# Performance work log

Measured on AMD Instinct MI355X. Metric: run time of the kernel, lower is better.

## Reference

```python
import jax, jax.numpy as jnp
import numpy as np

H = 64      # hidden_dim
NH = 4      # attention heads
HD = H // NH
NC = 13     # num_classes
NF = 8      # node features


def setup_inputs() -> dict:
    key = jax.random.key(0)
    ks = iter(jax.random.split(key, 32))
    B, T, N, E = 4, 16, 4096, 32768
    s = 0.05
    d = {}
    d["node_features"] = jax.random.normal(next(ks), (B, T, N, NF), jnp.float32)
    d["edge_index"] = jax.random.randint(next(ks), (T, 2, E), 0, N, jnp.int32)
    # spatial conv (Linear(NF,H), ReLU, Linear(H,H))
    d["sc_w1"] = jax.random.normal(next(ks), (H, NF), jnp.float32) * s
    d["sc_b1"] = jnp.zeros((H,), jnp.float32)
    d["sc_w2"] = jax.random.normal(next(ks), (H, H), jnp.float32) * s
    d["sc_b2"] = jnp.zeros((H,), jnp.float32)
    # 2-layer LSTM (pytorch gate order i,f,g,o)
    for l in range(2):
        d[f"lstm_w_ih{l}"] = jax.random.normal(next(ks), (4 * H, H), jnp.float32) * s
        d[f"lstm_w_hh{l}"] = jax.random.normal(next(ks), (4 * H, H), jnp.float32) * s
        d[f"lstm_b_ih{l}"] = jnp.zeros((4 * H,), jnp.float32)
        d[f"lstm_b_hh{l}"] = jnp.zeros((4 * H,), jnp.float32)
    # MultiheadAttention in_proj / out_proj
    d["attn_w_in"] = jax.random.normal(next(ks), (3 * H, H), jnp.float32) * s
    d["attn_b_in"] = jnp.zeros((3 * H,), jnp.float32)
    d["attn_w_out"] = jax.random.normal(next(ks), (H, H), jnp.float32) * s
    d["attn_b_out"] = jnp.zeros((H,), jnp.float32)
    # predictor MLP (dropout inactive at eval)
    d["p_w1"] = jax.random.normal(next(ks), (2 * H, H), jnp.float32) * s
    d["p_b1"] = jnp.zeros((2 * H,), jnp.float32)
    d["p_w2"] = jax.random.normal(next(ks), (H, 2 * H), jnp.float32) * s
    d["p_b2"] = jnp.zeros((H,), jnp.float32)
    d["p_w3"] = jax.random.normal(next(ks), (NC, H), jnp.float32) * s
    d["p_b3"] = jnp.zeros((NC,), jnp.float32)
    return d


def _lstm_layer(x, w_ih, w_hh, b_ih, b_hh):
    # x: (T, BN, H_in) -> (T, BN, H)
    BN = x.shape[1]
    Hh = w_hh.shape[1]

    def step(carry, xt):
        h, c = carry
        z = xt @ w_ih.T + h @ w_hh.T + (b_ih + b_hh)
        i, f, g, o = jnp.split(z, 4, axis=-1)
        c = jax.nn.sigmoid(f) * c + jax.nn.sigmoid(i) * jnp.tanh(g)
        h = jax.nn.sigmoid(o) * jnp.tanh(c)
        return (h, c), h

    h0 = jnp.zeros((BN, Hh), x.dtype)
    _, ys = jax.lax.scan(step, (h0, h0), x)
    return ys


def _forward(node_features, edge_index, sc_w1, sc_b1, sc_w2, sc_b2,
             lstm_w_ih0, lstm_w_hh0, lstm_b_ih0, lstm_b_hh0,
             lstm_w_ih1, lstm_w_hh1, lstm_b_ih1, lstm_b_hh1,
             attn_w_in, attn_b_in, attn_w_out, attn_b_out,
             p_w1, p_b1, p_w2, p_b2, p_w3, p_b3):
    B, T, N, _ = node_features.shape
    # spatial conv applied to every (b,t,n)
    h = jax.nn.relu(jnp.einsum('btnf,hf->btnh', node_features, sc_w1) + sc_b1)
    h = jnp.einsum('btnh,gh->btng', h, sc_w2) + sc_b2  # (B,T,N,H)

    def agg_step(_, inp):
        h_t, edges = inp  # (B,N,H), (2,E)
        src, dst = edges[0], edges[1]
        msgs = h_t[:, src]  # (B,E,H) gathered from pre-update h_t (matches torch)
        ssum = jax.vmap(lambda m: jax.ops.segment_sum(m, dst, num_segments=N))(msgs)
        cnt = jax.ops.segment_sum(jnp.ones(dst.shape, h_t.dtype), dst, num_segments=N)
        mean = ssum / jnp.maximum(cnt, 1.0)[None, :, None]
        h_new = jnp.where(cnt[None, :, None] > 0, (h_t + mean) * 0.5, h_t)
        return None, h_new

    _, h_agg = jax.lax.scan(agg_step, None, (h.transpose(1, 0, 2, 3), edge_index))
    h = h_agg.transpose(1, 0, 2, 3)  # (B,T,N,H)

    # per-node temporal sequence: (T, B*N, H)
    x = h.transpose(0, 2, 1, 3).reshape(B * N, T, H).transpose(1, 0, 2)
    x = _lstm_layer(x, lstm_w_ih0, lstm_w_hh0, lstm_b_ih0, lstm_b_hh0)
    x = _lstm_layer(x, lstm_w_ih1, lstm_w_hh1, lstm_b_ih1, lstm_b_hh1)
    x = x.transpose(1, 0, 2)  # (BN,T,H)

    # multi-head self-attention (batch_first)
    qkv = x @ attn_w_in.T + attn_b_in
    q, k, v = jnp.split(qkv, 3, axis=-1)
    BN = q.shape[0]
    q = q.reshape(BN, T, NH, HD)
    k = k.reshape(BN, T, NH, HD)
    v = v.reshape(BN, T, NH, HD)
    scores = jnp.einsum('bthd,bshd->bhts', q, k) / jnp.sqrt(jnp.float32(HD)).astype(x.dtype)
    attn = jax.nn.softmax(scores, axis=-1)
    o = jnp.einsum('bhts,bshd->bthd', attn, v).reshape(BN, T, H)
    o = o @ attn_w_out.T + attn_b_out

    final = o[:, -1, :]  # (BN,H)
    z = jax.nn.relu(final @ p_w1.T + p_b1)
    z = jax.nn.relu(z @ p_w2.T + p_b2)
    logits = z @ p_w3.T + p_b3
    return logits.reshape(B, N, NC)


def reference(node_features, edge_index, sc_w1, sc_b1, sc_w2, sc_b2,
              lstm_w_ih0, lstm_w_hh0, lstm_b_ih0, lstm_b_hh0,
              lstm_w_ih1, lstm_w_hh1, lstm_b_ih1, lstm_b_hh1,
              attn_w_in, attn_b_in, attn_w_out, attn_b_out,
              p_w1, p_b1, p_w2, p_b2, p_w3, p_b3):
    return _forward(node_features, edge_index, sc_w1, sc_b1, sc_w2, sc_b2,
                    lstm_w_ih0, lstm_w_hh0, lstm_b_ih0, lstm_b_hh0,
                    lstm_w_ih1, lstm_w_hh1, lstm_b_ih1, lstm_b_hh1,
                    attn_w_in, attn_b_in, attn_w_out, attn_b_out,
                    p_w1, p_b1, p_w2, p_b2, p_w3, p_b3)
```

## Files before the change

kernel.cpp:

```cpp
#include <hip/hip_runtime.h>

constexpr int kB  = 4;
constexpr int kT  = 16;
constexpr int kN  = 4096;
constexpr int kBN = kB * kN;
constexpr int kE  = 32768;
constexpr int kNC = 13;

typedef _Float16 f16x8 __attribute__((ext_vector_type(8)));
typedef _Float16 f16x4 __attribute__((ext_vector_type(4)));
typedef float f32x4 __attribute__((ext_vector_type(4)));

__device__ __forceinline__ float sigm(float x) { return 1.f / (1.f + __expf(-x)); }
__device__ __forceinline__ float tanh_(float x) {
  float e = __expf(2.f * x);
  return 1.f - 2.f / (e + 1.f);
}

__device__ __forceinline__ f32x4 mm3(f16x8 ah, f16x8 al, f16x8 bh, f16x8 bl, f32x4 acc) {
  acc = __builtin_amdgcn_mfma_f32_16x16x32_f16(ah, bh, acc, 0, 0, 0);
  acc = __builtin_amdgcn_mfma_f32_16x16x32_f16(ah, bl, acc, 0, 0, 0);
  acc = __builtin_amdgcn_mfma_f32_16x16x32_f16(al, bh, acc, 0, 0, 0);
  return acc;
}

__device__ __forceinline__ void split8(const float* p, f16x8& hi, f16x8& lo) {
  float4 u0 = *(const float4*)p, u1 = *(const float4*)(p + 4);
  float vv[8] = {u0.x, u0.y, u0.z, u0.w, u1.x, u1.y, u1.z, u1.w};
#pragma unroll
  for (int j = 0; j < 8; ++j) {
    _Float16 hj = (_Float16)vv[j];
    hi[j] = hj;
    lo[j] = (_Float16)(vv[j] - (float)hj);
  }
}

__device__ __forceinline__ void split8T(const float* base, int kbase, int seq,
                                        f16x8& hi, f16x8& lo) {
  float vv[8];
#pragma unroll
  for (int j = 0; j < 8; ++j) vv[j] = base[(kbase + j) * 68 + seq];
#pragma unroll
  for (int j = 0; j < 8; ++j) {
    _Float16 hj = (_Float16)vv[j];
    hi[j] = hj;
    lo[j] = (_Float16)(vv[j] - (float)hj);
  }
}

__device__ __forceinline__ unsigned int packf(float v) {
  _Float16 h = (_Float16)v;
  _Float16 l = (_Float16)(v - (float)h);
  unsigned short uh = __builtin_bit_cast(unsigned short, h);
  unsigned short ul = __builtin_bit_cast(unsigned short, l);
  return (unsigned int)uh | ((unsigned int)ul << 16);
}
__device__ __forceinline__ float up2(unsigned int w) {
  _Float16 h = __builtin_bit_cast(_Float16, (unsigned short)(w & 0xFFFFu));
  _Float16 l = __builtin_bit_cast(_Float16, (unsigned short)(w >> 16));
  return (float)h + (float)l;
}
__device__ __forceinline__ void unpack8(const unsigned int* w, f16x8& hi, f16x8& lo) {
#pragma unroll
  for (int j = 0; j < 8; ++j) {
    hi[j] = __builtin_bit_cast(_Float16, (unsigned short)(w[j] & 0xFFFFu));
    lo[j] = __builtin_bit_cast(_Float16, (unsigned short)(w[j] >> 16));
  }
}

__global__ __launch_bounds__(256, 2) void conv_kernel(
    const float* __restrict__ nf, const float* __restrict__ w1,
    const float* __restrict__ b1, const float* __restrict__ w2,
    const float* __restrict__ b2, unsigned int* __restrict__ hpk) {
  __shared__ unsigned int act[256 * 68];
  int tid = threadIdx.x;
  int w = tid >> 6, lane = tid & 63;
  int q = lane >> 4, i = lane & 15;
  int flat0 = blockIdx.x * 256;
  int bb = flat0 >> 16;
  int t = (flat0 >> 12) & 15;
  int n0 = flat0 & 4095;

  f16x8 w1h[4], w1l[4];
  f16x8 w2h[4][2], w2l[4][2];
  float bias1[4], bias2[4];
#pragma unroll
  for (int nt = 0; nt < 4; ++nt) {
    int n = nt * 16 + i;
    if (q == 0) split8(w1 + n * 8, w1h[nt], w1l[nt]);
    else { w1h[nt] = (f16x8)0; w1l[nt] = (f16x8)0; }
#pragma unroll
    for (int ks = 0; ks < 2; ++ks)
      split8(w2 + n * 64 + ks * 32 + q * 8, w2h[nt][ks], w2l[nt][ks]);
    bias1[nt] = b1[n];
    bias2[nt] = b2[n];
  }

  f16x8 xh[4], xl[4];
#pragma unroll
  for (int Mt = 0; Mt < 4; ++Mt) {
    if (q == 0)
      split8(nf + (size_t)(flat0 + w * 64 + Mt * 16 + i) * 8, xh[Mt], xl[Mt]);
    else { xh[Mt] = (f16x8)0; xl[Mt] = (f16x8)0; }
  }
#pragma unroll
  for (int Mt = 0; Mt < 4; ++Mt)
#pragma unroll
    for (int nt = 0; nt < 4; ++nt) {
      f32x4 acc = {bias1[nt], bias1[nt], bias1[nt], bias1[nt]};
      acc = mm3(xh[Mt], xl[Mt], w1h[nt], w1l[nt], acc);
#pragma unroll
      for (int r = 0; r < 4; ++r)
        act[(w * 64 + Mt * 16 + q * 4 + r) * 68 + nt * 16 + i] =
            packf(fmaxf(acc[r], 0.f));
    }
  __syncthreads();

  f32x4 acc2[4][4];
#pragma unroll
  for (int Mt = 0; Mt < 4; ++Mt)
#pragma unroll
    for (int nt = 0; nt < 4; ++nt) {
      acc2[Mt][nt][0] = bias2[nt]; acc2[Mt][nt][1] = bias2[nt];
      acc2[Mt][nt][2] = bias2[nt]; acc2[Mt][nt][3] = bias2[nt];
    }
#pragma unroll
  for (int ks = 0; ks < 2; ++ks)
#pragma unroll
    for (int Mt = 0; Mt < 4; ++Mt) {
      const unsigned int* p = &act[(w * 64 + Mt * 16 + i) * 68 + ks * 32 + q * 8];
      unsigned int wd[8];
#pragma unroll
      for (int j = 0; j < 4; ++j) {
        uint2 u = *(const uint2*)(p + j * 2);
        wd[2 * j] = u.x; wd[2 * j + 1] = u.y;
      }
      f16x8 ah, al;
      unpack8(wd, ah, al);
#pragma unroll
      for (int nt = 0; nt < 4; ++nt)
        acc2[Mt][nt] = mm3(ah, al, w2h[nt][ks], w2l[nt][ks], acc2[Mt][nt]);
    }
  __syncthreads();
#pragma unroll
  for (int Mt = 0; Mt < 4; ++Mt)
#pragma unroll
    for (int nt = 0; nt < 4; ++nt)
#pragma unroll
      for (int r = 0; r < 4; ++r)
        act[(w * 64 + Mt * 16 + q * 4 + r) * 68 + nt * 16 + i] =
            packf(acc2[Mt][nt][r]);
  __syncthreads();
  size_t tbase = ((size_t)t * kBN + (size_t)bb * kN + n0) * 64;
#pragma unroll
  for (int k = 0; k < 16; ++k) {
    int d0 = (k * 256 + tid) * 4;
    int node = d0 >> 6, ch = d0 & 63;
    uint2 a = *(const uint2*)&act[node * 68 + ch];
    uint2 b = *(const uint2*)&act[node * 68 + ch + 2];
    uint4 vv = {a.x, a.y, b.x, b.y};
    *(uint4*)(hpk + tbase + d0) = vv;
  }
}

__global__ __launch_bounds__(256) void count_kernel(
    const int* __restrict__ ei, int* __restrict__ cnt) {
  int i = blockIdx.x * 256 + threadIdx.x;
  int t = i >> 15, e = i & (kE - 1);
  int dst = ei[t * 2 * kE + kE + e];
  atomicAdd(&cnt[t * kN + dst], 1);
}

__global__ __launch_bounds__(1024) void scan_kernel(
    const int* __restrict__ cnt, int* __restrict__ off, int* __restrict__ cur) {
  __shared__ int sdata[1024];
  int t = blockIdx.x;
  int tid = threadIdx.x;
  const int* c = cnt + t * kN;
  int v0 = c[tid * 4], v1 = c[tid * 4 + 1], v2 = c[tid * 4 + 2], v3 = c[tid * 4 + 3];
  int s = v0 + v1 + v2 + v3;
  sdata[tid] = s;
  __syncthreads();
  for (int d = 1; d < 1024; d <<= 1) {
    int add = (tid >= d) ? sdata[tid - d] : 0;
    __syncthreads();
    sdata[tid] += add;
    __syncthreads();
  }
  int base = sdata[tid] - s;
  int o = t * kN + tid * 4;
  off[o] = base;            cur[o] = base;
  off[o + 1] = base + v0;   cur[o + 1] = base + v0;
  off[o + 2] = base + v0 + v1;        cur[o + 2] = base + v0 + v1;
  off[o + 3] = base + v0 + v1 + v2;   cur[o + 3] = base + v0 + v1 + v2;
}

__global__ __launch_bounds__(256) void place_kernel(
    const int* __restrict__ ei, int* __restrict__ cur, int* __restrict__ csr) {
  int i = blockIdx.x * 256 + threadIdx.x;
  int t = i >> 15, e = i & (kE - 1);
  int src = ei[t * 2 * kE + e];
  int dst = ei[t * 2 * kE + kE + e];
  int pos = atomicAdd(&cur[t * kN + dst], 1);
  csr[t * kE + pos] = src;
}

__global__ __launch_bounds__(256) void gather_kernel(
    const unsigned int* __restrict__ hpk, const int* __restrict__ csr,
    const int* __restrict__ off, const int* __restrict__ cnt,
    _Float16* __restrict__ xhi, _Float16* __restrict__ xlo) {
  int wv = blockIdx.x * 4 + (threadIdx.x >> 6);
  int t = wv >> 12, d = wv & (kN - 1);
  int lane = threadIdx.x & 63;
  int b = lane >> 4, cq = lane & 15;
  int o = off[t * kN + d];
  int c = cnt[t * kN + d];
  size_t tb = ((size_t)t * kBN + (size_t)b * kN) * 64 + cq * 4;
  const int* cs = csr + t * kE + o;
  float s[4] = {0.f, 0.f, 0.f, 0.f};
  int j = 0;
  for (; j + 4 <= c; j += 4) {
    int i0 = cs[j], i1 = cs[j + 1], i2 = cs[j + 2], i3 = cs[j + 3];
    uint4 v0 = *(const uint4*)(hpk + tb + (size_t)i0 * 64);
    uint4 v1 = *(const uint4*)(hpk + tb + (size_t)i1 * 64);
    uint4 v2 = *(const uint4*)(hpk + tb + (size_t)i2 * 64);
    uint4 v3 = *(const uint4*)(hpk + tb + (size_t)i3 * 64);
    s[0] += up2(v0.x) + up2(v1.x) + up2(v2.x) + up2(v3.x);
    s[1] += up2(v0.y) + up2(v1.y) + up2(v2.y) + up2(v3.y);
    s[2] += up2(v0.z) + up2(v1.z) + up2(v2.z) + up2(v3.z);
    s[3] += up2(v0.w) + up2(v1.w) + up2(v2.w) + up2(v3.w);
  }
  for (; j < c; ++j) {
    int i0 = cs[j];
    uint4 v0 = *(const uint4*)(hpk + tb + (size_t)i0 * 64);
    s[0] += up2(v0.x); s[1] += up2(v0.y); s[2] += up2(v0.z); s[3] += up2(v0.w);
  }
  uint4 hv = *(const uint4*)(hpk + tb + (size_t)d * 64);
  float hvf[4] = {up2(hv.x), up2(hv.y), up2(hv.z), up2(hv.w)};
  f16x4 ohi, olo;
  float inv = (c > 0) ? 1.f / (float)c : 0.f;
#pragma unroll
  for (int u = 0; u < 4; ++u) {
    float ov = (c > 0) ? (hvf[u] + s[u] * inv) * 0.5f : hvf[u];
    _Float16 hi = (_Float16)ov;
    ohi[u] = hi;
    olo[u] = (_Float16)(ov - (float)hi);
  }
  *(f16x4*)(xhi + tb + (size_t)d * 64) = ohi;
  *(f16x4*)(xlo + tb + (size_t)d * 64) = olo;
}

__global__ __launch_bounds__(256, 2) void lstm_kernel(
    const _Float16* __restrict__ xhi, const _Float16* __restrict__ xlo,
    _Float16* __restrict__ yhi, _Float16* __restrict__ ylo,
    const float* __restrict__ wih, const float* __restrict__ whh,
    const float* __restrict__ bih, const float* __restrict__ bhh) {
  __shared__ _Float16 hfrag[2][2][2][2][512];
  int tid = threadIdx.x;
  int cb = tid >> 6, lane = tid & 63;
  int q = lane >> 4, i = lane & 15;
  int s0 = blockIdx.x * 32;

  f16x8 wr[2][4][2][2];
#pragma unroll
  for (int mat = 0; mat < 2; ++mat) {
    const float* W = mat ? whh : wih;
#pragma unroll
    for (int g = 0; g < 4; ++g) {
      int row = (g * 4 + cb) * 16 + i;
#pragma unroll
      for (int ks = 0; ks < 2; ++ks)
        split8(W + row * 64 + ks * 32 + q * 8, wr[mat][g][ks][0], wr[mat][g][ks][1]);
    }
  }
  int ch = cb * 16 + i;
  float bias4[4];
#pragma unroll
  for (int g = 0; g < 4; ++g) bias4[g] = bih[g * 64 + ch] + bhh[g * 64 + ch];
  float cst[2][4];
#pragma unroll
  for (int ml = 0; ml < 2; ++ml)
#pragma unroll
    for (int r = 0; r < 4; ++r) cst[ml][r] = 0.f;
  int ks2 = ch >> 5, q2 = (ch >> 3) & 3, j2 = ch & 7;
  int p = 0;

  for (int t = 0; t < kT; ++t) {
    f32x4 acc[2][4];
#pragma unroll
    for (int ml = 0; ml < 2; ++ml)
#pragma unroll
      for (int g = 0; g < 4; ++g) {
        acc[ml][g][0] = bias4[g]; acc[ml][g][1] = bias4[g];
        acc[ml][g][2] = bias4[g]; acc[ml][g][3] = bias4[g];
      }
#pragma unroll
    for (int ks = 0; ks < 2; ++ks) {
      f16x8 xah[2], xal[2];
#pragma unroll
      for (int ml = 0; ml < 2; ++ml) {
        size_t base = ((size_t)t * kBN + s0 + ml * 16 + i) * 64 + ks * 32 + q * 8;
        xah[ml] = *(const f16x8*)(xhi + base);
        xal[ml] = *(const f16x8*)(xlo + base);
      }
#pragma unroll
      for (int g = 0; g < 4; ++g)
#pragma unroll
        for (int ml = 0; ml < 2; ++ml)
          acc[ml][g] = mm3(xah[ml], xal[ml], wr[0][g][ks][0], wr[0][g][ks][1], acc[ml][g]);
    }
    if (t > 0) {
#pragma unroll
      for (int ks = 0; ks < 2; ++ks) {
        f16x8 hah[2], hal[2];
#pragma unroll
        for (int ml = 0; ml < 2; ++ml) {
          hah[ml] = *(const f16x8*)&hfrag[p][ml][ks][0][lane * 8];
          hal[ml] = *(const f16x8*)&hfrag[p][ml][ks][1][lane * 8];
        }
#pragma unroll
        for (int g = 0; g < 4; ++g)
#pragma unroll
          for (int ml = 0; ml < 2; ++ml)
            acc[ml][g] = mm3(hah[ml], hal[ml], wr[1][g][ks][0], wr[1][g][ks][1], acc[ml][g]);
      }
    }
#pragma unroll
    for (int ml = 0; ml < 2; ++ml)
#pragma unroll
      for (int r = 0; r < 4; ++r) {
        float zi = acc[ml][0][r], zf = acc[ml][1][r];
        float zg = acc[ml][2][r], zo = acc[ml][3][r];
        float ig = sigm(zi), fg = sigm(zf), gg = tanh_(zg), og = sigm(zo);
        float c = fg * cst[ml][r] + ig * gg;
        cst[ml][r] = c;
        float hv = og * tanh_(c);
        int row = q * 4 + r;
        size_t ob = ((size_t)t * kBN + s0 + ml * 16 + row) * 64 + ch;
        _Float16 hh = (_Float16)hv;
        _Float16 hl = (_Float16)(hv - (float)hh);
        yhi[ob] = hh;
        ylo[ob] = hl;
        int lane2 = q2 * 16 + row;
        hfrag[p ^ 1][ml][ks2][0][lane2 * 8 + j2] = hh;
        hfrag[p ^ 1][ml][ks2][1][lane2 * 8 + j2] = hl;
      }
    __syncthreads();
    p ^= 1;
  }
}

__device__ __forceinline__ void stage_frags64(const float* W, _Float16* base,
                                              int O, int tid) {
  int total = O * 16;
  for (int idx = tid; idx < total; idx += 256) {
    int r = idx >> 4, k4 = idx & 15;
    float4 v = *(const float4*)&W[r * 64 + k4 * 4];
    int k = k4 * 4;
    int nt = r >> 4, ii = r & 15, ks = k >> 5, qq = (k >> 3) & 3, j0 = k & 7;
    _Float16* dh = base + ((nt * 2 + ks) * 2) * 512 + (qq * 16 + ii) * 8 + j0;
    _Float16* dl = dh + 512;
    float vv[4] = {v.x, v.y, v.z, v.w};
#pragma unroll
    for (int u = 0; u < 4; ++u) {
      _Float16 hh = (_Float16)vv[u];
      dh[u] = hh;
      dl[u] = (_Float16)(vv[u] - (float)hh);
    }
  }
}

__device__ __forceinline__ void stage_frags128(const float* W, _Float16* base,
                                               int O, int tid) {
  int total = O * 32;
  for (int idx = tid; idx < total; idx += 256) {
    int r = idx >> 5, k4 = idx & 31;
    float4 v = *(const float4*)&W[r * 128 + k4 * 4];
    int k = k4 * 4;
    int nt = r >> 4, ii = r & 15, ks = k >> 5, qq = (k >> 3) & 3, j0 = k & 7;
    _Float16* dh = base + ((nt * 4 + ks) * 2) * 512 + (qq * 16 + ii) * 8 + j0;
    _Float16* dl = dh + 512;
    float vv[4] = {v.x, v.y, v.z, v.w};
#pragma unroll
    for (int u = 0; u < 4; ++u) {
      _Float16 hh = (_Float16)vv[u];
      dh[u] = hh;
      dl[u] = (_Float16)(vv[u] - (float)hh);
    }
  }
}

__global__ __launch_bounds__(256, 1) void head_kernel(
    const _Float16* __restrict__ xhi, const _Float16* __restrict__ xlo,
    const float* __restrict__ win, const float* __restrict__ bin,
    const float* __restrict__ wout, const float* __restrict__ bout,
    const float* __restrict__ pw1, const float* __restrict__ pb1,
    const float* __restrict__ pw2, const float* __restrict__ pb2,
    const float* __restrict__ pw3, const float* __restrict__ pb3,
    float* __restrict__ out) {
  __shared__ __align__(16) float smem[30720];
  _Float16* wb = (_Float16*)smem;
  float* buf = smem + 21504;

  int tid = threadIdx.x;
  int w = tid >> 6, lane = tid & 63;
  int q = lane >> 4, i = lane & 15;
  int s0 = blockIdx.x * 64;

  stage_frags64(win, wb, 64, tid);
  stage_frags64(win + 64 * 64, wb + 8192, 128, tid);
  __syncthreads();

  {
    f16x8 ah[2], al[2];
#pragma unroll
    for (int ks = 0; ks < 2; ++ks) {
      size_t base = ((size_t)15 * kBN + s0 + w * 16 + i) * 64 + ks * 32 + q * 8;
      ah[ks] = *(const f16x8*)(xhi + base);
      al[ks] = *(const f16x8*)(xlo + base);
    }
#pragma unroll
    for (int nt = 0; nt < 4; ++nt) {
      float bias = bin[nt * 16 + i];
      f32x4 acc = {bias, bias, bias, bias};
#pragma unroll
      for (int ks = 0; ks < 2; ++ks) {
        const _Float16* bp = wb + ((nt * 2 + ks) * 2) * 512 + lane * 8;
        acc = mm3(ah[ks], al[ks], *(const f16x8*)bp, *(const f16x8*)(bp + 512), acc);
      }
      *(float4*)&buf[(nt * 16 + i) * 68 + w * 16 + q * 4] = *(float4*)&acc;
    }
  }
  __syncthreads();
  float qreg[16];
#pragma unroll
  for (int d = 0; d < 16; ++d) qreg[d] = buf[(w * 16 + d) * 68 + lane];
  __syncthreads();

  float m = -1e30f, l = 0.f;
  float o[16];
#pragma unroll
  for (int d = 0; d < 16; ++d) o[d] = 0.f;

  for (int t = 0; t < kT; ++t) {
    f16x8 xah[4][2], xal[4][2];
#pragma unroll
    for (int Mt = 0; Mt < 4; ++Mt)
#pragma unroll
      for (int ks = 0; ks < 2; ++ks) {
        size_t base = ((size_t)t * kBN + s0 + Mt * 16 + i) * 64 + ks * 32 + q * 8;
        xah[Mt][ks] = *(const f16x8*)(xhi + base);
        xal[Mt][ks] = *(const f16x8*)(xlo + base);
      }
#pragma unroll
    for (int u = 0; u < 2; ++u) {
      int nt = 2 * w + u;
      float bias = bin[64 + nt * 16 + i];
      f16x8 bh[2], bl[2];
#pragma unroll
      for (int ks = 0; ks < 2; ++ks) {
        const _Float16* bp = wb + 8192 + ((nt * 2 + ks) * 2) * 512 + lane * 8;
        bh[ks] = *(const f16x8*)bp;
        bl[ks] = *(const f16x8*)(bp + 512);
      }
#pragma unroll
      for (int Mt = 0; Mt < 4; ++Mt) {
        f32x4 acc = {bias, bias, bias, bias};
#pragma unroll
        for (int ks = 0; ks < 2; ++ks)
          acc = mm3(xah[Mt][ks], xal[Mt][ks], bh[ks], bl[ks], acc);
        *(float4*)&buf[(nt * 16 + i) * 68 + Mt * 16 + q * 4] = *(float4*)&acc;
      }
    }
    __syncthreads();
    float sc = 0.f;
#pragma unroll
    for (int d = 0; d < 16; ++d) sc += qreg[d] * buf[(w * 16 + d) * 68 + lane];
    sc *= 0.25f;
    float mn = fmaxf(m, sc);
    float alpha = __expf(m - mn);
    float pp = __expf(sc - mn);
    l = l * alpha + pp;
#pragma unroll
    for (int d = 0; d < 16; ++d)
      o[d] = o[d] * alpha + pp * buf[(64 + w * 16 + d) * 68 + lane];
    m = mn;
    __syncthreads();
  }

  float linv = 1.f / l;
#pragma unroll
  for (int d = 0; d < 16; ++d) buf[(w * 16 + d) * 68 + lane] = o[d] * linv;
  __syncthreads();

  stage_frags64(wout, wb, 64, tid);
  stage_frags64(pw1, wb + 8192, 128, tid);
  stage_frags128(pw2, wb + 24576, 64, tid);
  for (int idx = tid; idx < 256; idx += 256) {
    int r = idx >> 4, k4 = idx & 15;
    float4 v = {0.f, 0.f, 0.f, 0.f};
    if (r < kNC) v = *(const float4*)&pw3[r * 64 + k4 * 4];
    int k = k4 * 4;
    int ks = k >> 5, qq = (k >> 3) & 3, j0 = k & 7;
    _Float16* dh = wb + 40960 + (ks * 2) * 512 + (qq * 16 + r) * 8 + j0;
    _Float16* dl = dh + 512;
    float vv[4] = {v.x, v.y, v.z, v.w};
#pragma unroll
    for (int u = 0; u < 4; ++u) {
      _Float16 hh = (_Float16)vv[u];
      dh[u] = hh;
      dl[u] = (_Float16)(vv[u] - (float)hh);
    }
  }
  __syncthreads();

  int seq = w * 16 + i;

  {
    f16x8 ah[2], al[2];
    split8T(buf, q * 8, seq, ah[0], al[0]);
    split8T(buf, 32 + q * 8, seq, ah[1], al[1]);
#pragma unroll
    for (int nt = 0; nt < 4; ++nt) {
      float bias = bout[nt * 16 + i];
      f32x4 acc = {bias, bias, bias, bias};
#pragma unroll
      for (int ks = 0; ks < 2; ++ks) {
        const _Float16* bp = wb + ((nt * 2 + ks) * 2) * 512 + lane * 8;
        acc = mm3(ah[ks], al[ks], *(const f16x8*)bp, *(const f16x8*)(bp + 512), acc);
      }
      *(float4*)&buf[4352 + (nt * 16 + i) * 68 + w * 16 + q * 4] = *(float4*)&acc;
    }
  }
  __syncthreads();

  {
    f16x8 ah[2], al[2];
    split8T(buf + 4352, q * 8, seq, ah[0], al[0]);
    split8T(buf + 4352, 32 + q * 8, seq, ah[1], al[1]);
    __syncthreads();
#pragma unroll
    for (int nt = 0; nt < 8; ++nt) {
      float bias = pb1[nt * 16 + i];
      f32x4 acc = {bias, bias, bias, bias};
#pragma unroll
      for (int ks = 0; ks < 2; ++ks) {
        const _Float16* bp = wb + 8192 + ((nt * 2 + ks) * 2) * 512 + lane * 8;
        acc = mm3(ah[ks], al[ks], *(const f16x8*)bp, *(const f16x8*)(bp + 512), acc);
      }
      f32x4 r4;
#pragma unroll
      for (int r = 0; r < 4; ++r) r4[r] = fmaxf(acc[r], 0.f);
      *(float4*)&buf[(nt * 16 + i) * 68 + w * 16 + q * 4] = *(float4*)&r4;
    }
  }
  __syncthreads();

  {
    f16x8 ah[4], al[4];
#pragma unroll
    for (int ks = 0; ks < 4; ++ks)
      split8T(buf, ks * 32 + q * 8, seq, ah[ks], al[ks]);
    __syncthreads();
#pragma unroll
    for (int nt = 0; nt < 4; ++nt) {
      float bias = pb2[nt * 16 + i];
      f32x4 acc = {bias, bias, bias, bias};
#pragma unroll
      for (int ks = 0; ks < 4; ++ks) {
        const _Float16* bp = wb + 24576 + ((nt * 4 + ks) * 2) * 512 + lane * 8;
        acc = mm3(ah[ks], al[ks], *(const f16x8*)bp, *(const f16x8*)(bp + 512), acc);
      }
      f32x4 r4;
#pragma unroll
      for (int r = 0; r < 4; ++r) r4[r] = fmaxf(acc[r], 0.f);
      *(float4*)&buf[(nt * 16 + i) * 68 + w * 16 + q * 4] = *(float4*)&r4;
    }
  }
  __syncthreads();

  {
    f16x8 ah[2], al[2];
    split8T(buf, q * 8, seq, ah[0], al[0]);
    split8T(buf, 32 + q * 8, seq, ah[1], al[1]);
    f32x4 acc = {0.f, 0.f, 0.f, 0.f};
#pragma unroll
    for (int ks = 0; ks < 2; ++ks) {
      const _Float16* bp = wb + 40960 + (ks * 2) * 512 + lane * 8;
      acc = mm3(ah[ks], al[ks], *(const f16x8*)bp, *(const f16x8*)(bp + 512), acc);
    }
    if (i < kNC) {
      float bb = pb3[i];
#pragma unroll
      for (int r = 0; r < 4; ++r)
        out[(size_t)(s0 + w * 16 + q * 4 + r) * kNC + i] = acc[r] + bb;
    }
  }
}

extern "C" void kernel_launch(void* const* d_in, const int* in_sizes, int n_in,
                              void* d_out, int out_size, void* d_ws, size_t ws_size,
                              hipStream_t stream) {
  const float* nf    = (const float*)d_in[0];
  const int*   ei    = (const int*)d_in[1];
  const float* sc_w1 = (const float*)d_in[2];
  const float* sc_b1 = (const float*)d_in[3];
  const float* sc_w2 = (const float*)d_in[4];
  const float* sc_b2 = (const float*)d_in[5];
  const float* wih0  = (const float*)d_in[6];
  const float* whh0  = (const float*)d_in[7];
  const float* bih0  = (const float*)d_in[8];
  const float* bhh0  = (const float*)d_in[9];
  const float* wih1  = (const float*)d_in[10];
  const float* whh1  = (const float*)d_in[11];
  const float* bih1  = (const float*)d_in[12];
  const float* bhh1  = (const float*)d_in[13];
  const float* win   = (const float*)d_in[14];
  const float* bin   = (const float*)d_in[15];
  const float* wout  = (const float*)d_in[16];
  const float* bout  = (const float*)d_in[17];
  const float* pw1   = (const float*)d_in[18];
  const float* pb1   = (const float*)d_in[19];
  const float* pw2   = (const float*)d_in[20];
  const float* pb2   = (const float*)d_in[21];
  const float* pw3   = (const float*)d_in[22];
  const float* pb3   = (const float*)d_in[23];
  float* out = (float*)d_out;

  const size_t NB = (size_t)kT * kBN * 64;
  unsigned int* Hpk = (unsigned int*)d_ws;
  _Float16* Ahi = (_Float16*)(Hpk + NB);
  _Float16* Alo = Ahi + NB;
  _Float16* Bhi = Alo + NB;
  _Float16* Blo = Bhi + NB;
  int* cnt = (int*)(Blo + NB);
  int* off = cnt + kT * kN;
  int* cur = off + kT * kN;
  int* csr = cur + kT * kN;

  hipMemsetAsync(cnt, 0, (size_t)kT * kN * sizeof(int), stream);

  conv_kernel<<<1024, 256, 0, stream>>>(nf, sc_w1, sc_b1, sc_w2, sc_b2, Hpk);
  count_kernel<<<2048, 256, 0, stream>>>(ei, cnt);
  scan_kernel<<<16, 1024, 0, stream>>>(cnt, off, cur);
  place_kernel<<<2048, 256, 0, stream>>>(ei, cur, csr);
  gather_kernel<<<16384, 256, 0, stream>>>(Hpk, csr, off, cnt, Bhi, Blo);
  lstm_kernel<<<512, 256, 0, stream>>>(Bhi, Blo, Ahi, Alo, wih0, whh0, bih0, bhh0);
  lstm_kernel<<<512, 256, 0, stream>>>(Ahi, Alo, Bhi, Blo, wih1, whh1, bih1, bhh1);
  head_kernel<<<256, 256, 0, stream>>>(Bhi, Blo, win, bin, wout, bout,
                                       pw1, pb1, pw2, pb2, pw3, pb3, out);
}
```

Before: 464.5 us.

## Fuse both LSTM layers into one wavefront-pipelined kernel via shared memory

Replaces the two per-layer LSTM launches with a single kernel that runs layer 0 and layer 1 in separate 256-thread groups of a 512-thread block. Layer 1 consumes layer 0's hidden state from shared memory one timestep behind. This removes the global write and re-read of the intermediate layer-0 sequence and one kernel launch. The cost is larger blocks with more register pressure, one extra pipeline step, and a shared barrier that couples the two layers' step latency.

```diff
diff --git a/kernel.cpp b/kernel.cpp
--- a/kernel.cpp
+++ b/kernel.cpp
@@ -250,21 +250,30 @@
   *(f16x4*)(xlo + tb + (size_t)d * 64) = olo;
 }
 
-__global__ __launch_bounds__(256, 2) void lstm_kernel(
+__global__ __launch_bounds__(512, 2) void lstm2_kernel(
     const _Float16* __restrict__ xhi, const _Float16* __restrict__ xlo,
     _Float16* __restrict__ yhi, _Float16* __restrict__ ylo,
-    const float* __restrict__ wih, const float* __restrict__ whh,
-    const float* __restrict__ bih, const float* __restrict__ bhh) {
-  __shared__ _Float16 hfrag[2][2][2][2][512];
+    const float* __restrict__ wih0, const float* __restrict__ whh0,
+    const float* __restrict__ bih0, const float* __restrict__ bhh0,
+    const float* __restrict__ wih1, const float* __restrict__ whh1,
+    const float* __restrict__ bih1, const float* __restrict__ bhh1) {
+  __shared__ _Float16 h1f[2][2][2][2][512];
+  __shared__ _Float16 h2f[2][2][2][2][512];
   int tid = threadIdx.x;
-  int cb = tid >> 6, lane = tid & 63;
+  int grp = tid >> 8;
+  int cb = (tid >> 6) & 3, lane = tid & 63;
   int q = lane >> 4, i = lane & 15;
   int s0 = blockIdx.x * 32;
 
+  const float* Wih = grp ? wih1 : wih0;
+  const float* Whh = grp ? whh1 : whh0;
+  const float* Bih = grp ? bih1 : bih0;
+  const float* Bhh = grp ? bhh1 : bhh0;
+
   f16x8 wr[2][4][2][2];
 #pragma unroll
   for (int mat = 0; mat < 2; ++mat) {
-    const float* W = mat ? whh : wih;
+    const float* W = mat ? Whh : Wih;
 #pragma unroll
     for (int g = 0; g < 4; ++g) {
       int row = (g * 4 + cb) * 16 + i;
@@ -276,7 +285,7 @@
   int ch = cb * 16 + i;
   float bias4[4];
 #pragma unroll
-  for (int g = 0; g < 4; ++g) bias4[g] = bih[g * 64 + ch] + bhh[g * 64 + ch];
+  for (int g = 0; g < 4; ++g) bias4[g] = Bih[g * 64 + ch] + Bhh[g * 64 + ch];
   float cst[2][4];
 #pragma unroll
   for (int ml = 0; ml < 2; ++ml)
@@ -285,66 +294,130 @@
   int ks2 = ch >> 5, q2 = (ch >> 3) & 3, j2 = ch & 7;
   int p = 0;
 
-  for (int t = 0; t < kT; ++t) {
-    f32x4 acc[2][4];
-#pragma unroll
-    for (int ml = 0; ml < 2; ++ml)
-#pragma unroll
-      for (int g = 0; g < 4; ++g) {
-        acc[ml][g][0] = bias4[g]; acc[ml][g][1] = bias4[g];
-        acc[ml][g][2] = bias4[g]; acc[ml][g][3] = bias4[g];
-      }
-#pragma unroll
-    for (int ks = 0; ks < 2; ++ks) {
-      f16x8 xah[2], xal[2];
-#pragma unroll
-      for (int ml = 0; ml < 2; ++ml) {
-        size_t base = ((size_t)t * kBN + s0 + ml * 16 + i) * 64 + ks * 32 + q * 8;
-        xah[ml] = *(const f16x8*)(xhi + base);
-        xal[ml] = *(const f16x8*)(xlo + base);
-      }
-#pragma unroll
-      for (int g = 0; g < 4; ++g)
+  for (int it = 0; it < kT + 1; ++it) {
+    if (grp == 0) {
+      if (it < kT) {
+        int t = it;
+        f32x4 acc[2][4];
 #pragma unroll
         for (int ml = 0; ml < 2; ++ml)
-          acc[ml][g] = mm3(xah[ml], xal[ml], wr[0][g][ks][0], wr[0][g][ks][1], acc[ml][g]);
-    }
-    if (t > 0) {
-#pragma unroll
-      for (int ks = 0; ks < 2; ++ks) {
-        f16x8 hah[2], hal[2];
-#pragma unroll
-        for (int ml = 0; ml < 2; ++ml) {
-          hah[ml] = *(const f16x8*)&hfrag[p][ml][ks][0][lane * 8];
-          hal[ml] = *(const f16x8*)&hfrag[p][ml][ks][1][lane * 8];
+#pragma unroll
+          for (int g = 0; g < 4; ++g) {
+            acc[ml][g][0] = bias4[g]; acc[ml][g][1] = bias4[g];
+            acc[ml][g][2] = bias4[g]; acc[ml][g][3] = bias4[g];
+          }
+#pragma unroll
+        for (int ks = 0; ks < 2; ++ks) {
+          f16x8 xah[2], xal[2];
+#pragma unroll
+          for (int ml = 0; ml < 2; ++ml) {
+            size_t base = ((size_t)t * kBN + s0 + ml * 16 + i) * 64 + ks * 32 + q * 8;
+            xah[ml] = *(const f16x8*)(xhi + base);
+            xal[ml] = *(const f16x8*)(xlo + base);
+          }
+#pragma unroll
+          for (int g = 0; g < 4; ++g)
+#pragma unroll
+            for (int ml = 0; ml < 2; ++ml)
+              acc[ml][g] = mm3(xah[ml], xal[ml], wr[0][g][ks][0], wr[0][g][ks][1], acc[ml][g]);
         }
-#pragma unroll
-        for (int g = 0; g < 4; ++g)
-#pragma unroll
-          for (int ml = 0; ml < 2; ++ml)
-            acc[ml][g] = mm3(hah[ml], hal[ml], wr[1][g][ks][0], wr[1][g][ks][1], acc[ml][g]);
-      }
-    }
-#pragma unroll
-    for (int ml = 0; ml < 2; ++ml)
-#pragma unroll
-      for (int r = 0; r < 4; ++r) {
-        float zi = acc[ml][0][r], zf = acc[ml][1][r];
-        float zg = acc[ml][2][r], zo = acc[ml][3][r];
-        float ig = sigm(zi), fg = sigm(zf), gg = tanh_(zg), og = sigm(zo);
-        float c = fg * cst[ml][r] + ig * gg;
-        cst[ml][r] = c;
-        float hv = og * tanh_(c);
-        int row = q * 4 + r;
-        size_t ob = ((size_t)t * kBN + s0 + ml * 16 + row) * 64 + ch;
-        _Float16 hh = (_Float16)hv;
-        _Float16 hl = (_Float16)(hv - (float)hh);
-        yhi[ob] = hh;
-        ylo[ob] = hl;
-        int lane2 = q2 * 16 + row;
-        hfrag[p ^ 1][ml][ks2][0][lane2 * 8 + j2] = hh;
-        hfrag[p ^ 1][ml][ks2][1][lane2 * 8 + j2] = hl;
-      }
+        if (t > 0) {
+#pragma unroll
+          for (int ks = 0; ks < 2; ++ks) {
+            f16x8 hah[2], hal[2];
+#pragma unroll
+            for (int ml = 0; ml < 2; ++ml) {
+              hah[ml] = *(const f16x8*)&h1f[p][ml][ks][0][lane * 8];
+              hal[ml] = *(const f16x8*)&h1f[p][ml][ks][1][lane * 8];
+            }
+#pragma unroll
+            for (int g = 0; g < 4; ++g)
+#pragma unroll
+              for (int ml = 0; ml < 2; ++ml)
+                acc[ml][g] = mm3(hah[ml], hal[ml], wr[1][g][ks][0], wr[1][g][ks][1], acc[ml][g]);
+          }
+        }
+#pragma unroll
+        for (int ml = 0; ml < 2; ++ml)
+#pragma unroll
+          for (int r = 0; r < 4; ++r) {
+            float zi = acc[ml][0][r], zf = acc[ml][1][r];
+            float zg = acc[ml][2][r], zo = acc[ml][3][r];
+            float ig = sigm(zi), fg = sigm(zf), gg = tanh_(zg), og = sigm(zo);
+            float c = fg * cst[ml][r] + ig * gg;
+            cst[ml][r] = c;
+            float hv = og * tanh_(c);
+            int row = q * 4 + r;
+            _Float16 hh = (_Float16)hv;
+            _Float16 hl = (_Float16)(hv - (float)hh);
+            int lane2 = q2 * 16 + row;
+            h1f[p ^ 1][ml][ks2][0][lane2 * 8 + j2] = hh;
+            h1f[p ^ 1][ml][ks2][1][lane2 * 8 + j2] = hl;
+          }
+      }
+    } else {
+      if (it >= 1) {
+        int t = it - 1;
+        f32x4 acc[2][4];
+#pragma unroll
+        for (int ml = 0; ml < 2; ++ml)
+#pragma unroll
+          for (int g = 0; g < 4; ++g) {
+            acc[ml][g][0] = bias4[g]; acc[ml][g][1] = bias4[g];
+            acc[ml][g][2] = bias4[g]; acc[ml][g][3] = bias4[g];
+          }
+#pragma unroll
+        for (int ks = 0; ks < 2; ++ks) {
+          f16x8 xah[2], xal[2];
+#pragma unroll
+          for (int ml = 0; ml < 2; ++ml) {
+            xah[ml] = *(const f16x8*)&h1f[p][ml][ks][0][lane * 8];
+            xal[ml] = *(const f16x8*)&h1f[p][ml][ks][1][lane * 8];
+          }
+#pragma unroll
+          for (int g = 0; g < 4; ++g)
+#pragma unroll
+            for (int ml = 0; ml < 2; ++ml)
+              acc[ml][g] = mm3(xah[ml], xal[ml], wr[0][g][ks][0], wr[0][g][ks][1], acc[ml][g]);
+        }
+        if (t > 0) {
+#pragma unroll
+          for (int ks = 0; ks < 2; ++ks) {
+            f16x8 hah[2], hal[2];
+#pragma unroll
+            for (int ml = 0; ml < 2; ++ml) {
+              hah[ml] = *(const f16x8*)&h2f[p][ml][ks][0][lane * 8];
+              hal[ml] = *(const f16x8*)&h2f[p][ml][ks][1][lane * 8];
+            }
+#pragma unroll
+            for (int g = 0; g < 4; ++g)
+#pragma unroll
+              for (int ml = 0; ml < 2; ++ml)
+                acc[ml][g] = mm3(hah[ml], hal[ml], wr[1][g][ks][0], wr[1][g][ks][1], acc[ml][g]);
+          }
+        }
+#pragma unroll
+        for (int ml = 0; ml < 2; ++ml)
+#pragma unroll
+          for (int r = 0; r < 4; ++r) {
+            float zi = acc[ml][0][r], zf = acc[ml][1][r];
+            float zg = acc[ml][2][r], zo = acc[ml][3][r];
+            float ig = sigm(zi), fg = sigm(zf), gg = tanh_(zg), og = sigm(zo);
+            float c = fg * cst[ml][r] + ig * gg;
+            cst[ml][r] = c;
+            float hv = og * tanh_(c);
+            int row = q * 4 + r;
+            size_t ob = ((size_t)t * kBN + s0 + ml * 16 + row) * 64 + ch;
+            _Float16 hh = (_Float16)hv;
+            _Float16 hl = (_Float16)(hv - (float)hh);
+            yhi[ob] = hh;
+            ylo[ob] = hl;
+            int lane2 = q2 * 16 + row;
+            h2f[p ^ 1][ml][ks2][0][lane2 * 8 + j2] = hh;
+            h2f[p ^ 1][ml][ks2][1][lane2 * 8 + j2] = hl;
+          }
+      }
+    }
     __syncthreads();
     p ^= 1;
   }
@@ -645,8 +718,9 @@
   scan_kernel<<<16, 1024, 0, stream>>>(cnt, off, cur);
   place_kernel<<<2048, 256, 0, stream>>>(ei, cur, csr);
   gather_kernel<<<16384, 256, 0, stream>>>(Hpk, csr, off, cnt, Bhi, Blo);
-  lstm_kernel<<<512, 256, 0, stream>>>(Bhi, Blo, Ahi, Alo, wih0, whh0, bih0, bhh0);
-  lstm_kernel<<<512, 256, 0, stream>>>(Ahi, Alo, Bhi, Blo, wih1, whh1, bih1, bhh1);
-  head_kernel<<<256, 256, 0, stream>>>(Bhi, Blo, win, bin, wout, bout,
+  lstm2_kernel<<<512, 512, 0, stream>>>(Bhi, Blo, Ahi, Alo,
+                                        wih0, whh0, bih0, bhh0,
+                                        wih1, whh1, bih1, bhh1);
+  head_kernel<<<256, 256, 0, stream>>>(Ahi, Alo, win, bin, wout, bout,
                                        pw1, pb1, pw2, pb2, pw3, pb3, out);
 }
```

Result: faster. 452.3 us (-2.6%).
